# Optimization experiments

Measured on AMD Instinct MI355X. Metric: run time of the kernel, lower is better.

## Reference

```python
import jax, jax.numpy as jnp
import numpy as np

B, L1, L2, H = 8, 384, 384, 128


def _lin(k, out_f, in_f, scale=0.05):
    kw, kb = jax.random.split(k)
    return (jax.random.normal(kw, (out_f, in_f), jnp.float32) * scale,
            jax.random.normal(kb, (out_f,), jnp.float32) * scale)


def setup_inputs() -> dict:
    key = jax.random.key(0)
    ks = jax.random.split(key, 10)
    Wq_w, Wq_b = _lin(ks[2], H, H)
    Wup_w, Wup_b = _lin(ks[3], H, H)
    Wvp_w, Wvp_b = _lin(ks[4], H, H)
    V_w, V_b = _lin(ks[5], 1, H)
    Wg_w, Wg_b = _lin(ks[6], 2 * H, 2 * H)
    W_ih, b_ih = _lin(ks[7], 4 * H, 2 * H)
    W_hh, b_hh = _lin(ks[8], 4 * H, H)
    return {
        "x": jax.random.normal(ks[0], (B, L1, H), jnp.float32),
        "x_mask": jnp.zeros((B, L1), dtype=bool),
        "y": jax.random.normal(ks[1], (B, L2, H), jnp.float32),
        "y_mask": jnp.zeros((B, L2), dtype=bool),
        "Wq_w": Wq_w, "Wq_b": Wq_b,
        "Wup_w": Wup_w, "Wup_b": Wup_b,
        "Wvp_w": Wvp_w, "Wvp_b": Wvp_b,
        "V_w": V_w, "V_b": V_b,
        "Wg_w": Wg_w, "Wg_b": Wg_b,
        "W_ih": W_ih, "W_hh": W_hh, "b_ih": b_ih, "b_hh": b_hh,
    }


def reference(x, x_mask, y, y_mask, Wq_w, Wq_b, Wup_w, Wup_b, Wvp_w, Wvp_b,
              V_w, V_b, Wg_w, Wg_b, W_ih, W_hh, b_ih, b_hh):
    b, l1, h = x.shape
    # projections (torch Linear: x @ W.T + b)
    x_proj = x @ Wup_w.T + Wup_b                      # [B, L1, H]
    y_proj = y @ Wq_w.T + Wq_b                        # [B, L2, H]
    # source feeds a constant zero hidden state into W_vp -> just its bias
    hidden_proj = jnp.zeros((h,), x.dtype) @ Wvp_w.T + Wvp_b  # [H]
    # additive attention scores: V . tanh(xp + yp + hp)
    sum_batch = jnp.tanh(x_proj[:, :, None, :] + y_proj[:, None, :, :] + hidden_proj)  # [B,L1,L2,H]
    s = jnp.einsum('btjh,h->btj', sum_batch, V_w[0]) + V_b[0]  # [B, L1, L2]
    # sum_mask = (1 - x_mask) outer (1 - y_mask)
    xm = 1.0 - x_mask.astype(s.dtype)
    ym = 1.0 - y_mask.astype(s.dtype)
    s = s * (xm[:, :, None] * ym[:, None, :])
    s = jnp.where(y_mask[:, None, :], -jnp.inf, s)
    alpha = jax.nn.softmax(s, axis=-1)                # [B, L1, L2]
    ct = jnp.einsum('btj,bjh->bth', alpha, y)         # [B, L1, H]
    merge = jnp.concatenate([x, ct], axis=2)          # [B, L1, 2H]
    gt = jax.nn.sigmoid(merge @ Wg_w.T + Wg_b)
    lstm_in = gt * merge                              # [B, L1, 2H]
    # single-layer unidirectional LSTM (torch gate order: i, f, g, o)
    gates_x = lstm_in @ W_ih.T + b_ih                 # [B, L1, 4H]

    def step(carry, gx):
        h_t, c_t = carry
        g = gx + h_t @ W_hh.T + b_hh
        i, f, gg, o = jnp.split(g, 4, axis=-1)
        c_n = jax.nn.sigmoid(f) * c_t + jax.nn.sigmoid(i) * jnp.tanh(gg)
        h_n = jax.nn.sigmoid(o) * jnp.tanh(c_n)
        return (h_n, c_n), h_n

    init = (jnp.zeros((b, h), x.dtype), jnp.zeros((b, h), x.dtype))
    _, hs = jax.lax.scan(step, init, jnp.swapaxes(gates_x, 0, 1))  # [L1, B, H]
    return jnp.swapaxes(hs, 0, 1)                     # [B, L1, H]
```

## Files before the change

kernel.cpp:

```cpp
#include <hip/hip_runtime.h>
#include <hip/hip_bf16.h>
#include <math.h>

typedef __attribute__((ext_vector_type(4))) float  float4v;
typedef __attribute__((ext_vector_type(2))) float  float2v;
typedef __attribute__((ext_vector_type(8))) short  short8;

#define B_ 8
#define L_ 384
#define H_ 128

__device__ __forceinline__ float bflo(unsigned int u){ unsigned int t = u << 16; float f; __builtin_memcpy(&f,&t,4); return f; }
__device__ __forceinline__ unsigned short f2bf(float f){
  unsigned int t; __builtin_memcpy(&t,&f,4);
  return (unsigned short)((t + 0x7fffu + ((t>>16)&1u)) >> 16);
}
__device__ __forceinline__ float fsig(float x){ return __fdividef(1.f, 1.f + __expf(-x)); }

__device__ __forceinline__ void barrier_lds(){
  asm volatile("s_waitcnt lgkmcnt(0)\n\ts_barrier" ::: "memory");
}

template<int K>
__device__ __forceinline__ void mfma_rowgemm_body(
    unsigned short* in_s,
    const float* __restrict__ inA,
    const float* __restrict__ W, const float* __restrict__ bias,
    const float* __restrict__ bias2, float* __restrict__ out,
    int Ntotal, int act, int row0, int ob)
{
  constexpr int KP = K + 2;
  const int tid  = threadIdx.x;
  const int w    = tid >> 6;
  const int l    = tid & 63;
  const int c    = l & 15;
  const int quad = l >> 4;

  #pragma unroll
  for (int it = 0; it < K/32; ++it) {
    int idx = it*256 + tid;
    int r = idx / (K/4);
    int k = (idx % (K/4)) * 4;
    float4v f = *(const float4v*)(inA + (size_t)(row0+r)*K + k);
    unsigned int p0 = (unsigned int)f2bf(f.x) | ((unsigned int)f2bf(f.y) << 16);
    unsigned int p1 = (unsigned int)f2bf(f.z) | ((unsigned int)f2bf(f.w) << 16);
    *(unsigned int*)&in_s[r*KP + k]     = p0;
    *(unsigned int*)&in_s[r*KP + k + 2] = p1;
  }

  const int n = ob + w*16 + c;
  short8 bfr[K/32];
  #pragma unroll
  for (int kt = 0; kt < K/32; ++kt) {
    const float* src = W + (size_t)n*K + kt*32 + quad*8;
    float4v f0 = *(const float4v*)(src);
    float4v f1 = *(const float4v*)(src + 4);
    short8 v;
    v[0]=(short)f2bf(f0[0]); v[1]=(short)f2bf(f0[1]); v[2]=(short)f2bf(f0[2]); v[3]=(short)f2bf(f0[3]);
    v[4]=(short)f2bf(f1[0]); v[5]=(short)f2bf(f1[1]); v[6]=(short)f2bf(f1[2]); v[7]=(short)f2bf(f1[3]);
    bfr[kt] = v;
  }
  __syncthreads();

  const float4v z4 = {0.f,0.f,0.f,0.f};
  float4v acc0 = z4, acc1 = z4;
  #pragma unroll
  for (int kt = 0; kt < K/32; ++kt) {
    short8 a0 = *(const short8*)&in_s[(c     )*KP + kt*32 + quad*8];
    short8 a1 = *(const short8*)&in_s[(16 + c)*KP + kt*32 + quad*8];
    acc0 = __builtin_amdgcn_mfma_f32_16x16x32_bf16(a0, bfr[kt], acc0, 0,0,0);
    acc1 = __builtin_amdgcn_mfma_f32_16x16x32_bf16(a1, bfr[kt], acc1, 0,0,0);
  }

  const float C2 = 2.8853900817779268f;
  float bv = bias[n] + (bias2 ? bias2[n] : 0.f);
  #pragma unroll
  for (int mt = 0; mt < 2; ++mt) {
    float4v A = mt ? acc1 : acc0;
    #pragma unroll
    for (int r = 0; r < 4; ++r) {
      int m = mt*16 + quad*4 + r;
      float val = A[r] + bv;
      if (act == 4)
        val = __builtin_amdgcn_exp2f(C2 * val);
      if (act == 3)
        out[(size_t)(row0+m)*Ntotal + (n & 127)*4 + (n >> 7)] = val;
      else
        out[(size_t)(row0+m)*Ntotal + n] = val;
    }
  }
}

template<int K>
__global__ __launch_bounds__(256) void mfma_rowgemm_kernel(
    const float* __restrict__ inA,
    const float* __restrict__ W, const float* __restrict__ bias,
    const float* __restrict__ bias2, float* __restrict__ out,
    int Ntotal, int act)
{
  __shared__ __align__(16) unsigned short in_s[32*(K+2)];
  mfma_rowgemm_body<K>(in_s, inA, W, bias, bias2, out,
                       Ntotal, act, blockIdx.x*32, blockIdx.y*64);
}

__global__ __launch_bounds__(256) void proj_mfma_kernel(
    const float* __restrict__ x, const float* __restrict__ y,
    const float* __restrict__ Wup_w, const float* __restrict__ Wup_b,
    const float* __restrict__ Wq_w, const float* __restrict__ Wq_b,
    const float* __restrict__ Wvp_b,
    float* __restrict__ xp, float* __restrict__ yp)
{
  __shared__ __align__(16) unsigned short in_s[32*130];
  int bx = blockIdx.x;
  if (bx < 192)
    mfma_rowgemm_body<128>(in_s, x, Wup_w, Wup_b, nullptr,
                           xp, 128, 4, (bx>>1)*32, (bx&1)*64);
  else {
    bx -= 192;
    mfma_rowgemm_body<128>(in_s, y, Wq_w, Wq_b, Wvp_b,
                           yp, 128, 4, (bx>>1)*32, (bx&1)*64);
  }
}

__global__ __launch_bounds__(256) void attn_kernel(
    const float* __restrict__ xp, const float* __restrict__ yp,
    const float* __restrict__ y, const unsigned char* __restrict__ xmask,
    const unsigned char* __restrict__ ymask, const float* __restrict__ Vw,
    const float* __restrict__ Vb,
    float* __restrict__ ctpbase, float* __restrict__ ml)
{
  __shared__ __align__(16) float xp_s[8][128];
  __shared__ __align__(16) float v2_s[128];
  __shared__ __align__(16) float yp_s[32][132];
  __shared__ __align__(16) unsigned short p_s[16][40];
  __shared__ float sc_s[16];
  __shared__ float xm_s[8];
  __shared__ float ym_s[32];
  __shared__ float sv_s;
  const int tid = threadIdx.x;
  const int b   = blockIdx.y;
  const int t0  = blockIdx.x * 8;
  const int jh  = blockIdx.z;
  const int jb  = jh * 96;
  const int w    = tid >> 6;
  const int l    = tid & 63;
  const int c16  = l & 15;
  const int quad = l >> 4;
  {
    int r = tid >> 5, k4 = (tid & 31) * 4;
    float4v f = *(const float4v*)(xp + ((size_t)(b*L_ + t0 + r))*H_ + k4);
    *(float4v*)&xp_s[r][k4] = f;
    if (tid < 32) {
      float4v v = *(const float4v*)(Vw + tid*4);
      float4v v2; v2[0]=2.f*v[0]; v2[1]=2.f*v[1]; v2[2]=2.f*v[2]; v2[3]=2.f*v[3];
      *(float4v*)&v2_s[tid*4] = v2;
    }
    if (tid < 8) xm_s[tid] = xmask[b*L_ + t0 + tid] ? 0.f : 1.f;
    if (tid < 16) sc_s[tid] = 0.f;
    for (int i = 320 + tid; i < 640; i += 256) ((unsigned short*)p_s)[i] = 0;
  }
  __syncthreads();
  if (tid < 32) {
    float4v v = *(const float4v*)&v2_s[tid*4];
    float sm = (v[0]+v[1]) + (v[2]+v[3]);
    #pragma unroll
    for (int off = 16; off >= 1; off >>= 1) sm += __shfl_xor(sm, off);
    if (tid == 0) sv_s = 0.5f*sm + Vb[0];
  }

  float4v rp[4];
  unsigned char ymb = 0;
  {
    #pragma unroll
    for (int it = 0; it < 4; ++it) {
      int idx = it*256 + tid; int r = idx >> 5; int k4 = (idx & 31) * 4;
      rp[it] = *(const float4v*)(yp + ((size_t)(b*L_ + jb + r))*H_ + k4);
    }
    if (tid < 32) ymb = ymask[b*L_ + jb + tid];
  }

  const int t = tid >> 5, u = tid & 31;
  float mrun = -__builtin_inff(), lrun = 0.f;
  const float4v z4 = {0.f,0.f,0.f,0.f};
  float4v acc0 = z4, acc1 = z4;
  float svc = 0.f, xmv = 0.f;

  for (int c = 0; c < 3; ++c) {
    __syncthreads();
    #pragma unroll
    for (int it = 0; it < 4; ++it) {
      int idx = it*256 + tid; int r = idx >> 5; int k4 = (idx & 31) * 4;
      *(float4v*)&yp_s[r][k4] = rp[it];
    }
    if (tid < 32) ym_s[tid] = ymb ? 0.f : 1.f;
    __syncthreads();
    if (c == 0) { svc = sv_s; xmv = xm_s[t]; }
    short8 yb0, yb1;
    {
      const float* ybase = y + ((size_t)(b*L_ + jb + c*32 + quad*8))*H_ + c16;
      #pragma unroll
      for (int jj = 0; jj < 8; ++jj) {
        yb0[jj] = (short)f2bf(ybase[(size_t)jj*H_ + w*16]);
        yb1[jj] = (short)f2bf(ybase[(size_t)jj*H_ + (w+4)*16]);
      }
    }
    if (c < 2) {
      #pragma unroll
      for (int it = 0; it < 4; ++it) {
        int idx = it*256 + tid; int r = idx >> 5; int k4 = (idx & 31) * 4;
        rp[it] = *(const float4v*)(yp + ((size_t)(b*L_ + jb + (c+1)*32 + r))*H_ + k4);
      }
      if (tid < 32) ymb = ymask[b*L_ + jb + (c+1)*32 + tid];
    }

    float sA = 0.f, sB = 0.f;
    {
      const float* yr = yp_s[u];
      const float* xr = xp_s[t];
      #pragma unroll 4
      for (int k = 0; k < 128; k += 4) {
        float4v yv = *(const float4v*)&yr[k];
        float4v xv = *(const float4v*)&xr[k];
        float4v vv = *(const float4v*)&v2_s[k];
        sA -= vv[0] * __builtin_amdgcn_rcpf(__builtin_fmaf(xv[0], yv[0], 1.f));
        sB -= vv[1] * __builtin_amdgcn_rcpf(__builtin_fmaf(xv[1], yv[1], 1.f));
        sA -= vv[2] * __builtin_amdgcn_rcpf(__builtin_fmaf(xv[2], yv[2], 1.f));
        sB -= vv[3] * __builtin_amdgcn_rcpf(__builtin_fmaf(xv[3], yv[3], 1.f));
      }
    }
    float ymv = ym_s[u];
    float s = (svc + sA + sB) * xmv * ymv;
    if (ymv == 0.f) s = -__builtin_inff();
    float mc = s;
    #pragma unroll
    for (int off = 16; off >= 1; off >>= 1) mc = fmaxf(mc, __shfl_xor(mc, off));
    float mnew = fmaxf(mrun, mc);
    float p  = __expf(s - mnew);
    float sc = __expf(mrun - mnew);
    float ps = p;
    #pragma unroll
    for (int off = 16; off >= 1; off >>= 1) ps += __shfl_xor(ps, off);
    lrun = lrun * sc + ps;
    mrun = mnew;
    p_s[t][u] = f2bf(p);
    if (u == 0) sc_s[t] = sc;
    __syncthreads();
    short8 pf = *(const short8*)&p_s[c16][quad*8];
    float4v scv;
    #pragma unroll
    for (int r = 0; r < 4; ++r) scv[r] = sc_s[quad*4 + r];
    acc0 *= scv; acc1 *= scv;
    acc0 = __builtin_amdgcn_mfma_f32_16x16x32_bf16(pf, yb0, acc0, 0,0,0);
    acc1 = __builtin_amdgcn_mfma_f32_16x16x32_bf16(pf, yb1, acc1, 0,0,0);
  }
  float* ctp = ctpbase + (size_t)jh*393216;
  if (quad < 2) {
    #pragma unroll
    for (int r = 0; r < 4; ++r) {
      int row = b*L_ + t0 + quad*4 + r;
      ctp[(size_t)row*H_ + w*16 + c16]     = acc0[r];
      ctp[(size_t)row*H_ + (w+4)*16 + c16] = acc1[r];
    }
  }
  if (u == 0) {
    int row = b*L_ + t0 + t;
    ml[(jh*2+0)*3072 + row] = mrun;
    ml[(jh*2+1)*3072 + row] = lrun;
  }
}

__global__ __launch_bounds__(256) void gate1_kernel(
    const float* __restrict__ x,
    const float* __restrict__ ctpbase, const float* __restrict__ ml,
    const float* __restrict__ Wg_w, const float* __restrict__ Wg_b,
    float* __restrict__ out)
{
  constexpr int K = 256, KP = 258;
  __shared__ __align__(16) unsigned short in_s[32*KP];
  const int tid  = threadIdx.x;
  const int w    = tid >> 6;
  const int l    = tid & 63;
  const int c    = l & 15;
  const int quad = l >> 4;
  const int row0 = blockIdx.x * 32;
  const int ob   = blockIdx.y * 64;

  #pragma unroll
  for (int it = 0; it < 8; ++it) {
    int idx = it*256 + tid;
    int r = idx >> 6;
    int k = (idx & 63) * 4;
    int row = row0 + r;
    float4v f;
    if (k < 128) {
      f = *(const float4v*)(x + (size_t)row*128 + k);
    } else {
      float m0 = ml[       row], l0 = ml[  3072 + row];
      float m1 = ml[2*3072+row], l1 = ml[3*3072 + row];
      float m2 = ml[4*3072+row], l2 = ml[5*3072 + row];
      float m3 = ml[6*3072+row], l3 = ml[7*3072 + row];
      float mm = fmaxf(fmaxf(m0, m1), fmaxf(m2, m3));
      float e0 = __expf(m0-mm), e1 = __expf(m1-mm);
      float e2 = __expf(m2-mm), e3 = __expf(m3-mm);
      float inv = __fdividef(1.f, (l0*e0 + l1*e1) + (l2*e2 + l3*e3));
      size_t off = (size_t)row*128 + (k-128);
      float4v v0 = *(const float4v*)(ctpbase             + off);
      float4v v1 = *(const float4v*)(ctpbase +   393216  + off);
      float4v v2 = *(const float4v*)(ctpbase + 2*393216  + off);
      float4v v3 = *(const float4v*)(ctpbase + 3*393216  + off);
      f[0] = ((v0[0]*e0 + v1[0]*e1) + (v2[0]*e2 + v3[0]*e3))*inv;
      f[1] = ((v0[1]*e0 + v1[1]*e1) + (v2[1]*e2 + v3[1]*e3))*inv;
      f[2] = ((v0[2]*e0 + v1[2]*e1) + (v2[2]*e2 + v3[2]*e3))*inv;
      f[3] = ((v0[3]*e0 + v1[3]*e1) + (v2[3]*e2 + v3[3]*e3))*inv;
    }
    unsigned int p0 = (unsigned int)f2bf(f[0]) | ((unsigned int)f2bf(f[1]) << 16);
    unsigned int p1 = (unsigned int)f2bf(f[2]) | ((unsigned int)f2bf(f[3]) << 16);
    *(unsigned int*)&in_s[r*KP + k]     = p0;
    *(unsigned int*)&in_s[r*KP + k + 2] = p1;
  }

  const int n = ob + w*16 + c;
  short8 bfr[8];
  #pragma unroll
  for (int kt = 0; kt < 8; ++kt) {
    const float* src = Wg_w + (size_t)n*K + kt*32 + quad*8;
    float4v f0 = *(const float4v*)(src);
    float4v f1 = *(const float4v*)(src + 4);
    short8 v;
    v[0]=(short)f2bf(f0[0]); v[1]=(short)f2bf(f0[1]); v[2]=(short)f2bf(f0[2]); v[3]=(short)f2bf(f0[3]);
    v[4]=(short)f2bf(f1[0]); v[5]=(short)f2bf(f1[1]); v[6]=(short)f2bf(f1[2]); v[7]=(short)f2bf(f1[3]);
    bfr[kt] = v;
  }
  __syncthreads();

  const float4v z4 = {0.f,0.f,0.f,0.f};
  float4v acc0 = z4, acc1 = z4;
  #pragma unroll
  for (int kt = 0; kt < 8; ++kt) {
    short8 a0 = *(const short8*)&in_s[(c     )*KP + kt*32 + quad*8];
    short8 a1 = *(const short8*)&in_s[(16 + c)*KP + kt*32 + quad*8];
    acc0 = __builtin_amdgcn_mfma_f32_16x16x32_bf16(a0, bfr[kt], acc0, 0,0,0);
    acc1 = __builtin_amdgcn_mfma_f32_16x16x32_bf16(a1, bfr[kt], acc1, 0,0,0);
  }

  float bv = Wg_b[n];
  #pragma unroll
  for (int mt = 0; mt < 2; ++mt) {
    float4v A = mt ? acc1 : acc0;
    #pragma unroll
    for (int r = 0; r < 4; ++r) {
      int m = mt*16 + quad*4 + r;
      float val = A[r] + bv;
      float mg = bflo((unsigned int)in_s[m*KP + n]);
      out[(size_t)(row0+m)*256 + n] = fsig(val) * mg;
    }
  }
}

__global__ __launch_bounds__(512) void lstm_kernel(
    const float* __restrict__ gx, const float* __restrict__ Whh,
    float* __restrict__ out)
{
  __shared__ __align__(16) unsigned short h_s[2][128];
  const int tid  = threadIdx.x;
  const int b    = blockIdx.x;
  const int w    = tid >> 6;
  const int l    = tid & 63;
  const int col  = l & 15;
  const int quad = l >> 4;

  short8 bf[4][4];
  #pragma unroll
  for (int nt = 0; nt < 4; ++nt) {
    const int n = nt*128 + w*16 + col;
    #pragma unroll
    for (int kt = 0; kt < 4; ++kt) {
      const int k0 = kt*32 + quad*8;
      const float* src = Whh + (size_t)n*H_ + k0;
      float4v f0 = *(const float4v*)(src);
      float4v f1 = *(const float4v*)(src + 4);
      short8 v;
      v[0]=(short)f2bf(f0[0]); v[1]=(short)f2bf(f0[1]); v[2]=(short)f2bf(f0[2]); v[3]=(short)f2bf(f0[3]);
      v[4]=(short)f2bf(f1[0]); v[5]=(short)f2bf(f1[1]); v[6]=(short)f2bf(f1[2]); v[7]=(short)f2bf(f1[3]);
      bf[nt][kt] = v;
    }
  }

  if (tid < 128) { h_s[0][tid] = 0; h_s[1][tid] = 0; }
  float cst = 0.f;
  const int goff = w*16 + col;
  const float* gbase = gx + (size_t)b*L_*512 + goff*4;
  float* outp = out + (size_t)b*L_*H_ + goff;
  float4v gbuf[4];
  #pragma unroll
  for (int s = 0; s < 4; ++s)
    gbuf[s] = *(const float4v*)(gbase + (size_t)s*512);
  const float4v z4 = {0.f,0.f,0.f,0.f};
  const float NL2E = -1.4426950408889634f;
  const float P2L2E = 2.8853900817779268f;
  __syncthreads();

  for (int t4 = 0; t4 < L_; t4 += 4) {
    #pragma unroll
    for (int s = 0; s < 4; ++s) {
      const int tstep = t4 + s;
      const unsigned short* hb = h_s[s & 1];
      short8 a0 = *(const short8*)&hb[ 0 + quad*8];
      short8 a1 = *(const short8*)&hb[32 + quad*8];
      short8 a2 = *(const short8*)&hb[64 + quad*8];
      short8 a3 = *(const short8*)&hb[96 + quad*8];
      float4v gcur = gbuf[s];
      if (tstep + 4 < L_)
        gbuf[s] = *(const float4v*)(gbase + (size_t)(tstep+4)*512);
      float4v c2 = __builtin_amdgcn_mfma_f32_16x16x32_bf16(a0, bf[2][0], z4, 0,0,0);
      float4v c0 = __builtin_amdgcn_mfma_f32_16x16x32_bf16(a0, bf[0][0], z4, 0,0,0);
      c2 = __builtin_amdgcn_mfma_f32_16x16x32_bf16(a1, bf[2][1], c2, 0,0,0);
      c0 = __builtin_amdgcn_mfma_f32_16x16x32_bf16(a1, bf[0][1], c0, 0,0,0);
      c2 = __builtin_amdgcn_mfma_f32_16x16x32_bf16(a2, bf[2][2], c2, 0,0,0);
      c0 = __builtin_amdgcn_mfma_f32_16x16x32_bf16(a2, bf[0][2], c0, 0,0,0);
      c2 = __builtin_amdgcn_mfma_f32_16x16x32_bf16(a3, bf[2][3], c2, 0,0,0);
      c0 = __builtin_amdgcn_mfma_f32_16x16x32_bf16(a3, bf[0][3], c0, 0,0,0);
      float gg = 1.f - 2.f*__builtin_amdgcn_rcpf(
                   __builtin_amdgcn_exp2f(P2L2E*(c2[0] + gcur[2])) + 1.f);
      float ig = __builtin_amdgcn_rcpf(
                   1.f + __builtin_amdgcn_exp2f(NL2E*(c0[0] + gcur[0])));
      float4v c1 = __builtin_amdgcn_mfma_f32_16x16x32_bf16(a0, bf[1][0], z4, 0,0,0);
      float4v c3 = __builtin_amdgcn_mfma_f32_16x16x32_bf16(a0, bf[3][0], z4, 0,0,0);
      float igg = ig * gg;
      c1 = __builtin_amdgcn_mfma_f32_16x16x32_bf16(a1, bf[1][1], c1, 0,0,0);
      c3 = __builtin_amdgcn_mfma_f32_16x16x32_bf16(a1, bf[3][1], c3, 0,0,0);
      c1 = __builtin_amdgcn_mfma_f32_16x16x32_bf16(a2, bf[1][2], c1, 0,0,0);
      c3 = __builtin_amdgcn_mfma_f32_16x16x32_bf16(a2, bf[3][2], c3, 0,0,0);
      c1 = __builtin_amdgcn_mfma_f32_16x16x32_bf16(a3, bf[1][3], c1, 0,0,0);
      c3 = __builtin_amdgcn_mfma_f32_16x16x32_bf16(a3, bf[3][3], c3, 0,0,0);
      float fg = __builtin_amdgcn_rcpf(
                   1.f + __builtin_amdgcn_exp2f(NL2E*(c1[0] + gcur[1])));
      float og = __builtin_amdgcn_rcpf(
                   1.f + __builtin_amdgcn_exp2f(NL2E*(c3[0] + gcur[3])));
      cst = fg*cst + igg;
      float hn = og * (1.f - 2.f*__builtin_amdgcn_rcpf(
                   __builtin_amdgcn_exp2f(P2L2E*cst) + 1.f));
      if (quad == 0) {
        outp[(size_t)tstep*H_] = hn;
        h_s[(s+1)&1][goff] = f2bf(hn);
      }
      barrier_lds();
    }
  }
}

extern "C" void kernel_launch(void* const* d_in, const int* in_sizes, int n_in,
                              void* d_out, int out_size, void* d_ws, size_t ws_size,
                              hipStream_t stream)
{
  (void)in_sizes; (void)n_in; (void)out_size; (void)ws_size;
  const float* x     = (const float*)d_in[0];
  const unsigned char* xm = (const unsigned char*)d_in[1];
  const float* y     = (const float*)d_in[2];
  const unsigned char* ym = (const unsigned char*)d_in[3];
  const float* Wq_w  = (const float*)d_in[4];
  const float* Wq_b  = (const float*)d_in[5];
  const float* Wup_w = (const float*)d_in[6];
  const float* Wup_b = (const float*)d_in[7];
  const float* Wvp_b = (const float*)d_in[9];
  const float* V_w   = (const float*)d_in[10];
  const float* V_b   = (const float*)d_in[11];
  const float* Wg_w  = (const float*)d_in[12];
  const float* Wg_b  = (const float*)d_in[13];
  const float* W_ih  = (const float*)d_in[14];
  const float* W_hh  = (const float*)d_in[15];
  const float* b_ih  = (const float*)d_in[16];
  const float* b_hh  = (const float*)d_in[17];
  float* out = (float*)d_out;

  float* wsf    = (float*)d_ws;
  float* xp_ws  = wsf;
  float* yp_ws  = xp_ws + 393216;
  float* li_ws  = xp_ws;
  float* ctp_ws = yp_ws + 393216;
  float* gx_ws  = ctp_ws + 4*393216;
  float* ml_ws  = gx_ws + 1572864;

  proj_mfma_kernel<<<dim3(384),256,0,stream>>>(x, y, Wup_w, Wup_b, Wq_w, Wq_b, Wvp_b, xp_ws, yp_ws);
  attn_kernel<<<dim3(48,8,4),256,0,stream>>>(xp_ws, yp_ws, y, xm, ym, V_w, V_b, ctp_ws, ml_ws);
  gate1_kernel<<<dim3(96,4),256,0,stream>>>(x, ctp_ws, ml_ws, Wg_w, Wg_b, li_ws);
  mfma_rowgemm_kernel<256><<<dim3(96,8),256,0,stream>>>(li_ws, W_ih, b_ih, b_hh, gx_ws, 512, 3);
  lstm_kernel<<<dim3(8),512,0,stream>>>(gx_ws, W_hh, out);
}
```

Baseline: 332.2 us.

## Replace MFMA recurrent matvec in LSTM with fp16 dot2 and DPP reductions

The LSTM recurrence kernel no longer uses bf16 MFMA tiles for the per-step h·W_hh product, where only one row of each 16-row tile was useful. Each thread now owns one hidden unit and a quarter of the K dimension, holds fp16 weights in registers, and accumulates with v_dot2 instructions. The four partial sums are combined with DPP lane shuffles. This targets the MFMA latency on the serial critical path, at the cost of more VALU instructions per step and a switch from bf16 to fp16 for h and W_hh.

```diff
diff --git a/kernel.cpp b/kernel.cpp
--- a/kernel.cpp
+++ b/kernel.cpp
@@ -5,6 +5,8 @@
 typedef __attribute__((ext_vector_type(4))) float  float4v;
 typedef __attribute__((ext_vector_type(2))) float  float2v;
 typedef __attribute__((ext_vector_type(8))) short  short8;
+typedef __attribute__((ext_vector_type(2))) _Float16 half2v;
+typedef __attribute__((ext_vector_type(4))) unsigned int uint4v;
 
 #define B_ 8
 #define L_ 384
@@ -19,6 +21,31 @@
 
 __device__ __forceinline__ void barrier_lds(){
   asm volatile("s_waitcnt lgkmcnt(0)\n\ts_barrier" ::: "memory");
+}
+
+#if __has_builtin(__builtin_amdgcn_fdot2)
+__device__ __forceinline__ float fdot2(half2v a, half2v b, float c){
+  return __builtin_amdgcn_fdot2(a, b, c, false);
+}
+#else
+__device__ __forceinline__ float fdot2(half2v a, half2v b, float c){
+  return (float)a[0]*(float)b[0] + ((float)a[1]*(float)b[1] + c);
+}
+#endif
+
+__device__ __forceinline__ half2v u2h2(unsigned int u){ half2v h; __builtin_memcpy(&h,&u,4); return h; }
+
+__device__ __forceinline__ float dpp_xor1_add(float x){
+  int xi; __builtin_memcpy(&xi,&x,4);
+  int y = __builtin_amdgcn_update_dpp(0, xi, 0xB1, 0xF, 0xF, true);
+  float f; __builtin_memcpy(&f,&y,4);
+  return x + f;
+}
+__device__ __forceinline__ float dpp_xor2_add(float x){
+  int xi; __builtin_memcpy(&xi,&x,4);
+  int y = __builtin_amdgcn_update_dpp(0, xi, 0x4E, 0xF, 0xF, true);
+  float f; __builtin_memcpy(&f,&y,4);
+  return x + f;
 }
 
 template<int K>
@@ -362,87 +389,81 @@
     float* __restrict__ out)
 {
   __shared__ __align__(16) unsigned short h_s[2][128];
-  const int tid  = threadIdx.x;
-  const int b    = blockIdx.x;
-  const int w    = tid >> 6;
-  const int l    = tid & 63;
-  const int col  = l & 15;
-  const int quad = l >> 4;
-
-  short8 bf[4][4];
-  #pragma unroll
-  for (int nt = 0; nt < 4; ++nt) {
-    const int n = nt*128 + w*16 + col;
-    #pragma unroll
-    for (int kt = 0; kt < 4; ++kt) {
-      const int k0 = kt*32 + quad*8;
-      const float* src = Whh + (size_t)n*H_ + k0;
-      float4v f0 = *(const float4v*)(src);
-      float4v f1 = *(const float4v*)(src + 4);
-      short8 v;
-      v[0]=(short)f2bf(f0[0]); v[1]=(short)f2bf(f0[1]); v[2]=(short)f2bf(f0[2]); v[3]=(short)f2bf(f0[3]);
-      v[4]=(short)f2bf(f1[0]); v[5]=(short)f2bf(f1[1]); v[6]=(short)f2bf(f1[2]); v[7]=(short)f2bf(f1[3]);
-      bf[nt][kt] = v;
-    }
-  }
-
-  if (tid < 128) { h_s[0][tid] = 0; h_s[1][tid] = 0; }
+  const int tid = threadIdx.x;
+  const int b   = blockIdx.x;
+  const int j   = tid >> 2;
+  const int kq  = tid & 3;
+
+  half2v wreg[4][16];
+  #pragma unroll
+  for (int g = 0; g < 4; ++g) {
+    const float* src = Whh + ((size_t)(g*128 + j))*H_ + kq*32;
+    #pragma unroll
+    for (int i = 0; i < 8; ++i) {
+      float4v f = *(const float4v*)(src + i*4);
+      half2v lo, hi;
+      lo[0] = (_Float16)f[0]; lo[1] = (_Float16)f[1];
+      hi[0] = (_Float16)f[2]; hi[1] = (_Float16)f[3];
+      wreg[g][i*2]   = lo;
+      wreg[g][i*2+1] = hi;
+    }
+  }
+
+  if (tid < 256) ((unsigned short*)h_s)[tid] = 0;
+
   float cst = 0.f;
-  const int goff = w*16 + col;
-  const float* gbase = gx + (size_t)b*L_*512 + goff*4;
-  float* outp = out + (size_t)b*L_*H_ + goff;
+  const float* gbase = gx + (size_t)b*L_*512 + j*4;
+  float* outp = out + (size_t)b*L_*H_ + j;
   float4v gbuf[4];
   #pragma unroll
   for (int s = 0; s < 4; ++s)
     gbuf[s] = *(const float4v*)(gbase + (size_t)s*512);
-  const float4v z4 = {0.f,0.f,0.f,0.f};
-  const float NL2E = -1.4426950408889634f;
-  const float P2L2E = 2.8853900817779268f;
+  const float NL2E  = -1.4426950408889634f;
+  const float P2L2E =  2.8853900817779268f;
   __syncthreads();
 
   for (int t4 = 0; t4 < L_; t4 += 4) {
     #pragma unroll
     for (int s = 0; s < 4; ++s) {
       const int tstep = t4 + s;
-      const unsigned short* hb = h_s[s & 1];
-      short8 a0 = *(const short8*)&hb[ 0 + quad*8];
-      short8 a1 = *(const short8*)&hb[32 + quad*8];
-      short8 a2 = *(const short8*)&hb[64 + quad*8];
-      short8 a3 = *(const short8*)&hb[96 + quad*8];
+      const unsigned int* hp = (const unsigned int*)h_s[s & 1] + kq*16;
+      uint4v hq[4];
+      hq[0] = *(const uint4v*)(hp);
+      hq[1] = *(const uint4v*)(hp + 4);
+      hq[2] = *(const uint4v*)(hp + 8);
+      hq[3] = *(const uint4v*)(hp + 12);
       float4v gcur = gbuf[s];
       if (tstep + 4 < L_)
         gbuf[s] = *(const float4v*)(gbase + (size_t)(tstep+4)*512);
-      float4v c2 = __builtin_amdgcn_mfma_f32_16x16x32_bf16(a0, bf[2][0], z4, 0,0,0);
-      float4v c0 = __builtin_amdgcn_mfma_f32_16x16x32_bf16(a0, bf[0][0], z4, 0,0,0);
-      c2 = __builtin_amdgcn_mfma_f32_16x16x32_bf16(a1, bf[2][1], c2, 0,0,0);
-      c0 = __builtin_amdgcn_mfma_f32_16x16x32_bf16(a1, bf[0][1], c0, 0,0,0);
-      c2 = __builtin_amdgcn_mfma_f32_16x16x32_bf16(a2, bf[2][2], c2, 0,0,0);
-      c0 = __builtin_amdgcn_mfma_f32_16x16x32_bf16(a2, bf[0][2], c0, 0,0,0);
-      c2 = __builtin_amdgcn_mfma_f32_16x16x32_bf16(a3, bf[2][3], c2, 0,0,0);
-      c0 = __builtin_amdgcn_mfma_f32_16x16x32_bf16(a3, bf[0][3], c0, 0,0,0);
+      float a0 = 0.f, a1 = 0.f, a2 = 0.f, a3 = 0.f;
+      #pragma unroll
+      for (int d = 0; d < 16; ++d) {
+        half2v h2 = u2h2(hq[d>>2][d&3]);
+        a0 = fdot2(wreg[0][d], h2, a0);
+        a1 = fdot2(wreg[1][d], h2, a1);
+        a2 = fdot2(wreg[2][d], h2, a2);
+        a3 = fdot2(wreg[3][d], h2, a3);
+      }
+      a0 = dpp_xor2_add(dpp_xor1_add(a0));
+      a1 = dpp_xor2_add(dpp_xor1_add(a1));
+      a2 = dpp_xor2_add(dpp_xor1_add(a2));
+      a3 = dpp_xor2_add(dpp_xor1_add(a3));
+      float ig = __builtin_amdgcn_rcpf(
+                   1.f + __builtin_amdgcn_exp2f(NL2E*(a0 + gcur[0])));
+      float fg = __builtin_amdgcn_rcpf(
+                   1.f + __builtin_amdgcn_exp2f(NL2E*(a1 + gcur[1])));
       float gg = 1.f - 2.f*__builtin_amdgcn_rcpf(
-                   __builtin_amdgcn_exp2f(P2L2E*(c2[0] + gcur[2])) + 1.f);
-      float ig = __builtin_amdgcn_rcpf(
-                   1.f + __builtin_amdgcn_exp2f(NL2E*(c0[0] + gcur[0])));
-      float4v c1 = __builtin_amdgcn_mfma_f32_16x16x32_bf16(a0, bf[1][0], z4, 0,0,0);
-      float4v c3 = __builtin_amdgcn_mfma_f32_16x16x32_bf16(a0, bf[3][0], z4, 0,0,0);
-      float igg = ig * gg;
-      c1 = __builtin_amdgcn_mfma_f32_16x16x32_bf16(a1, bf[1][1], c1, 0,0,0);
-      c3 = __builtin_amdgcn_mfma_f32_16x16x32_bf16(a1, bf[3][1], c3, 0,0,0);
-      c1 = __builtin_amdgcn_mfma_f32_16x16x32_bf16(a2, bf[1][2], c1, 0,0,0);
-      c3 = __builtin_amdgcn_mfma_f32_16x16x32_bf16(a2, bf[3][2], c3, 0,0,0);
-      c1 = __builtin_amdgcn_mfma_f32_16x16x32_bf16(a3, bf[1][3], c1, 0,0,0);
-      c3 = __builtin_amdgcn_mfma_f32_16x16x32_bf16(a3, bf[3][3], c3, 0,0,0);
-      float fg = __builtin_amdgcn_rcpf(
-                   1.f + __builtin_amdgcn_exp2f(NL2E*(c1[0] + gcur[1])));
+                   __builtin_amdgcn_exp2f(P2L2E*(a2 + gcur[2])) + 1.f);
       float og = __builtin_amdgcn_rcpf(
-                   1.f + __builtin_amdgcn_exp2f(NL2E*(c3[0] + gcur[3])));
-      cst = fg*cst + igg;
+                   1.f + __builtin_amdgcn_exp2f(NL2E*(a3 + gcur[3])));
+      cst = fg*cst + ig*gg;
       float hn = og * (1.f - 2.f*__builtin_amdgcn_rcpf(
                    __builtin_amdgcn_exp2f(P2L2E*cst) + 1.f));
-      if (quad == 0) {
+      if (kq == 0) {
         outp[(size_t)tstep*H_] = hn;
-        h_s[(s+1)&1][goff] = f2bf(hn);
+        _Float16 hh = (_Float16)hn;
+        unsigned short hb16; __builtin_memcpy(&hb16, &hh, 2);
+        h_s[(s+1)&1][j] = hb16;
       }
       barrier_lds();
     }
```

After: 366.8 us. 10.4% more time.
